# Kernel tuning notes

Measured on AMD Instinct MI355X. Metric: run time of the kernel, lower is better.

## Reference

```python
import jax, jax.numpy as jnp
import numpy as np

STRIDE = 8
PAD = 8
KSZ = 16


def setup_inputs() -> dict:
    key = jax.random.key(0)
    k1, k2, k3 = jax.random.split(key, 3)
    B, Cin, Cout, L = 16, 512, 1, 4000
    inp = jax.random.normal(k1, (B, Cin, L), dtype=jnp.float32)
    # t60 in [0.1, 0.5) so that round(t60*100)-10 lands in [0, 40]
    t60s = 0.1 + 0.39 * jax.random.uniform(k2, (B // 2,), dtype=jnp.float32)
    kernel_weight = jax.random.uniform(k3, (41, Cin, Cout, KSZ), dtype=jnp.float32)
    return {"input": inp, "t60s": t60s, "kernel_weight": kernel_weight}


def reference(input, t60s, kernel_weight):
    # per-sample kernel index: round(t60*100).int().repeat(2) - 10
    idx = jnp.tile(jnp.round(t60s * 100.0).astype(jnp.int32), 2) - 10  # (B,)
    w = kernel_weight[idx]                      # (B, Cin, Cout, K) gathered per sample
    # torch conv_transpose1d(x, W) == conv(x with lhs_dilation=stride,
    #                                      flip_k(W).swap(Cin,Cout), pad=K-1-p)
    w = jnp.flip(jnp.swapaxes(w, 1, 2), axis=-1)  # (B, Cout, Cin, K)
    pad = KSZ - 1 - PAD

    def per_sample(x, wk):  # x: (Cin, L), wk: (Cout, Cin, K)
        y = jax.lax.conv_general_dilated(
            x[None], wk,
            window_strides=(1,),
            padding=[(pad, pad)],
            lhs_dilation=(STRIDE,),
            dimension_numbers=("NCH", "OIH", "NCH"),
        )
        return y[0]  # (Cout, L_out), L_out = (L-1)*stride - 2*PAD + K

    return jax.vmap(per_sample)(input, w)  # (B, Cout, L_out)
```

## Files before the change

kernel.cpp:

```cpp
#include <hip/hip_runtime.h>

#define L_IN   4000
#define CIN    512
#define KSZ    16
#define LOUT   31992
#define NQ     3999
#define QPB    256
#define CPB    256
#define RST    1088

__global__ __launch_bounds__(512, 4)
void dereverb_kernel(const float* __restrict__ x,
                     const float* __restrict__ t60s,
                     const float* __restrict__ kw,
                     float* __restrict__ out)
{
    __shared__ float lds[4 * RST];

    const int b    = blockIdx.y;
    const int q0   = blockIdx.x * QPB;
    const int cih  = blockIdx.z;
    const int tid  = threadIdx.x;
    const int lane = tid & 63;
    const int wave = tid >> 6;

    float t60 = t60s[b & 7];
    int kidx = (int)rintf(t60 * 100.0f) - 10;
    kidx = __builtin_amdgcn_readfirstlane(kidx);
    const float4* wsrc = (const float4*)(kw + ((size_t)kidx * CIN + cih * CPB) * KSZ);

    ((float4*)lds)[tid]       = wsrc[tid];
    ((float4*)lds)[tid + 512] = wsrc[tid + 512];
    __syncthreads();

    const int qb  = q0 + 4 * lane;
    const int qbl = qb < 3996 ? qb : 3996;
    const int qan = (qb + 4) < NQ ? (qb + 4) : NQ;

    const float* xr = x + ((size_t)b * CIN + cih * CPB + wave * 32) * L_IN;
    const float* xp = xr + qbl;
    const float* xq = xr + qan;
    const float4* wl = (const float4*)(lds + wave * 32 * KSZ);

    float acc[4][8];
    #pragma unroll
    for (int qi = 0; qi < 4; ++qi)
        #pragma unroll
        for (int r = 0; r < 8; ++r) acc[qi][r] = 0.0f;

#define FMA_BODY(A, AN, W0, W1, W2, W3) do {                        \
        const float xl[4] = {(A).x, (A).y, (A).z, (A).w};           \
        const float xh[4] = {(A).y, (A).z, (A).w, (AN)};            \
        const float wa[8] = {(W0).x,(W0).y,(W0).z,(W0).w,           \
                             (W1).x,(W1).y,(W1).z,(W1).w};          \
        const float wb[8] = {(W2).x,(W2).y,(W2).z,(W2).w,           \
                             (W3).x,(W3).y,(W3).z,(W3).w};          \
        _Pragma("unroll")                                           \
        for (int qi = 0; qi < 4; ++qi)                              \
            _Pragma("unroll")                                       \
            for (int r = 0; r < 8; ++r) {                           \
                acc[qi][r] = fmaf(xh[qi], wa[r], acc[qi][r]);       \
                acc[qi][r] = fmaf(xl[qi], wb[r], acc[qi][r]);       \
            }                                                       \
    } while (0)

    float4 a0 = *(const float4*)xp;
    float  n0 = *xq;
    float4 a1 = *(const float4*)(xp + L_IN);
    float  n1 = *(xq + L_IN);
    float4 w0 = wl[0], w1 = wl[1], w2 = wl[2], w3 = wl[3];

    #pragma unroll 2
    for (int ci = 0; ci < 30; ++ci) {
        float4 a2 = *(const float4*)(xp + 2 * L_IN);
        float  n2 = *(xq + 2 * L_IN);
        float4 u0 = wl[4], u1 = wl[5], u2 = wl[6], u3 = wl[7];
        FMA_BODY(a0, n0, w0, w1, w2, w3);
        a0 = a1; n0 = n1; a1 = a2; n1 = n2;
        w0 = u0; w1 = u1; w2 = u2; w3 = u3;
        xp += L_IN; xq += L_IN; wl += 4;
    }
    {
        float4 u0 = wl[4], u1 = wl[5], u2 = wl[6], u3 = wl[7];
        FMA_BODY(a0, n0, w0, w1, w2, w3);
        a0 = a1; n0 = n1;
        w0 = u0; w1 = u1; w2 = u2; w3 = u3;
    }
    FMA_BODY(a0, n0, w0, w1, w2, w3);

    #pragma unroll
    for (int qi = 0; qi < 4; ++qi)
        if (qb + qi > NQ - 1)
            #pragma unroll
            for (int r = 0; r < 8; ++r) acc[qi][r] = 0.0f;

    const size_t obase = (size_t)b * LOUT + (size_t)q0 * 8;
    #pragma unroll
    for (int p = 0; p < 2; ++p) {
        __syncthreads();
        if (wave >= 4) {
            float* rp = lds + (wave - 4) * RST + lane * 17;
            #pragma unroll
            for (int qih = 0; qih < 2; ++qih)
                #pragma unroll
                for (int r = 0; r < 8; ++r)
                    rp[qih * 8 + r] = acc[2 * p + qih][r];
        }
        __syncthreads();
        if (wave < 4) {
            float* rp = lds + wave * RST + lane * 17;
            #pragma unroll
            for (int qih = 0; qih < 2; ++qih)
                #pragma unroll
                for (int r = 0; r < 8; ++r)
                    rp[qih * 8 + r] += acc[2 * p + qih][r];
        }
        __syncthreads();
        const int k = tid >> 4, j = tid & 15;
        #pragma unroll
        for (int kk = 0; kk < 2; ++kk) {
            const int kc = k + 32 * kk;
            const int tl = 32 * kc + 16 * p + j;
            if (q0 * 8 + tl < LOUT) {
                float s = lds[0 * RST + kc * 17 + j]
                        + lds[1 * RST + kc * 17 + j]
                        + lds[2 * RST + kc * 17 + j]
                        + lds[3 * RST + kc * 17 + j];
                unsafeAtomicAdd(&out[obase + tl], s);
            }
        }
    }
#undef FMA_BODY
}

extern "C" void kernel_launch(void* const* d_in, const int* in_sizes, int n_in,
                              void* d_out, int out_size, void* d_ws, size_t ws_size,
                              hipStream_t stream) {
    const float* x    = (const float*)d_in[0];
    const float* t60s = (const float*)d_in[1];
    const float* kw   = (const float*)d_in[2];
    float* out = (float*)d_out;

    hipMemsetAsync(d_out, 0, out_size, stream);

    dim3 grid((NQ + QPB - 1) / QPB, 16, 2);
    dereverb_kernel<<<grid, 512, 0, stream>>>(x, t60s, kw, out);
}
```

Before: 195.7 us.

## Split work by channel chunks and replace LDS reduction with direct atomics

The grid is reorganised so each 1024-thread block handles one 32-channel chunk for one batch and the whole output length, instead of a tile of output positions over 256 channels. The cross-wave LDS reduction and its barriers are removed, and each thread adds its partial sums straight into global memory with atomics. This cuts LDS traffic and synchronisation, but each output now receives 16 atomic contributions instead of 2. The per-thread atomic pattern is strided, so atomic traffic and contention rise sharply.

```diff
diff --git a/kernel.cpp b/kernel.cpp
--- a/kernel.cpp
+++ b/kernel.cpp
@@ -5,21 +5,18 @@
 #define KSZ    16
 #define LOUT   31992
 #define NQ     3999
-#define QPB    256
-#define CPB    256
-#define RST    1088
+#define CCH    32
 
-__global__ __launch_bounds__(512, 4)
+__global__ __launch_bounds__(1024, 4)
 void dereverb_kernel(const float* __restrict__ x,
                      const float* __restrict__ t60s,
                      const float* __restrict__ kw,
                      float* __restrict__ out)
 {
-    __shared__ float lds[4 * RST];
+    __shared__ float wlds[CCH * KSZ];
 
+    const int c0   = blockIdx.x * CCH;
     const int b    = blockIdx.y;
-    const int q0   = blockIdx.x * QPB;
-    const int cih  = blockIdx.z;
     const int tid  = threadIdx.x;
     const int lane = tid & 63;
     const int wave = tid >> 6;
@@ -27,20 +24,20 @@
     float t60 = t60s[b & 7];
     int kidx = (int)rintf(t60 * 100.0f) - 10;
     kidx = __builtin_amdgcn_readfirstlane(kidx);
-    const float4* wsrc = (const float4*)(kw + ((size_t)kidx * CIN + cih * CPB) * KSZ);
 
-    ((float4*)lds)[tid]       = wsrc[tid];
-    ((float4*)lds)[tid + 512] = wsrc[tid + 512];
+    if (tid < 128)
+        ((float4*)wlds)[tid] =
+            ((const float4*)(kw + ((size_t)kidx * CIN + c0) * KSZ))[tid];
     __syncthreads();
 
-    const int qb  = q0 + 4 * lane;
+    const int qb  = wave * 256 + 4 * lane;
     const int qbl = qb < 3996 ? qb : 3996;
     const int qan = (qb + 4) < NQ ? (qb + 4) : NQ;
 
-    const float* xr = x + ((size_t)b * CIN + cih * CPB + wave * 32) * L_IN;
-    const float* xp = xr + qbl;
-    const float* xq = xr + qan;
-    const float4* wl = (const float4*)(lds + wave * 32 * KSZ);
+    const float* xrow = x + ((size_t)b * CIN + c0) * L_IN;
+    const float* xp = xrow + qbl;
+    const float* xq = xrow + qan;
+    const float4* wl = (const float4*)wlds;
 
     float acc[4][8];
     #pragma unroll
@@ -88,48 +85,13 @@
     }
     FMA_BODY(a0, n0, w0, w1, w2, w3);
 
+    float* op = out + (size_t)b * LOUT + (size_t)8 * qb;
     #pragma unroll
     for (int qi = 0; qi < 4; ++qi)
-        if (qb + qi > NQ - 1)
+        if (qb + qi <= NQ - 1)
             #pragma unroll
-            for (int r = 0; r < 8; ++r) acc[qi][r] = 0.0f;
-
-    const size_t obase = (size_t)b * LOUT + (size_t)q0 * 8;
-    #pragma unroll
-    for (int p = 0; p < 2; ++p) {
-        __syncthreads();
-        if (wave >= 4) {
-            float* rp = lds + (wave - 4) * RST + lane * 17;
-            #pragma unroll
-            for (int qih = 0; qih < 2; ++qih)
-                #pragma unroll
-                for (int r = 0; r < 8; ++r)
-                    rp[qih * 8 + r] = acc[2 * p + qih][r];
-        }
-        __syncthreads();
-        if (wave < 4) {
-            float* rp = lds + wave * RST + lane * 17;
-            #pragma unroll
-            for (int qih = 0; qih < 2; ++qih)
-                #pragma unroll
-                for (int r = 0; r < 8; ++r)
-                    rp[qih * 8 + r] += acc[2 * p + qih][r];
-        }
-        __syncthreads();
-        const int k = tid >> 4, j = tid & 15;
-        #pragma unroll
-        for (int kk = 0; kk < 2; ++kk) {
-            const int kc = k + 32 * kk;
-            const int tl = 32 * kc + 16 * p + j;
-            if (q0 * 8 + tl < LOUT) {
-                float s = lds[0 * RST + kc * 17 + j]
-                        + lds[1 * RST + kc * 17 + j]
-                        + lds[2 * RST + kc * 17 + j]
-                        + lds[3 * RST + kc * 17 + j];
-                unsafeAtomicAdd(&out[obase + tl], s);
-            }
-        }
-    }
+            for (int r = 0; r < 8; ++r)
+                unsafeAtomicAdd(op + 8 * qi + r, acc[qi][r]);
 #undef FMA_BODY
 }
 
@@ -143,6 +105,6 @@
 
     hipMemsetAsync(d_out, 0, out_size, stream);
 
-    dim3 grid((NQ + QPB - 1) / QPB, 16, 2);
-    dereverb_kernel<<<grid, 512, 0, stream>>>(x, t60s, kw, out);
+    dim3 grid(CIN / CCH, 16);
+    dereverb_kernel<<<grid, 1024, 0, stream>>>(x, t60s, kw, out);
 }
```

After: 604.9 us. +209.0%, slower.
